# Kernel optimization log

Measured on AMD Instinct MI355X. Metric: run time of the kernel, lower is better.

The kernel has to match this reference:

```python
import jax, jax.numpy as jnp
import numpy as np

N = 50000  # nodes (spots)


def setup_inputs() -> dict:
    key = jax.random.key(0)
    ks = jax.random.split(key, 10)
    d_gene, d_img, H, Hh, O = 3000, 1024, 512, 256, 64

    def lin(k, i, o):
        return (jax.random.normal(k, (i, o), jnp.float32) / np.sqrt(i).astype(np.float32))

    return {
        "gene_data": jax.random.normal(ks[0], (N, d_gene), jnp.float32),
        "image_data": jax.random.normal(ks[1], (N, d_img), jnp.float32),
        "gene_edge_index": jax.random.randint(ks[2], (2, 800000), 0, N, dtype=jnp.int32).astype(jnp.int64),
        "spatial_edge_index": jax.random.randint(ks[3], (2, 300000), 0, N, dtype=jnp.int32).astype(jnp.int64),
        "W_fc1": lin(ks[4], d_gene, H), "b_fc1": jnp.zeros((H,), jnp.float32),
        "W_fc2": lin(ks[5], d_img, H), "b_fc2": jnp.zeros((H,), jnp.float32),
        "W_g11": lin(ks[6], H, Hh), "b_g11": jnp.zeros((Hh,), jnp.float32),
        "W_g12": lin(ks[7], H, Hh), "b_g12": jnp.zeros((Hh,), jnp.float32),
        "W_g21": lin(ks[8], Hh, O), "b_g21": jnp.zeros((O,), jnp.float32),
        "W_g22": lin(ks[9], Hh, O), "b_g22": jnp.zeros((O,), jnp.float32),
        "w1": jnp.float32(0.5), "w2": jnp.float32(0.5),
    }


def _gcn(x, edge_index, W, b, n):
    # PyG GCNConv: h = x @ W; add self-loops; symmetric norm D^-1/2 (A+I) D^-1/2; scatter-add; + bias
    h = x @ W  # [n, out]
    loop = jnp.arange(n, dtype=edge_index.dtype)
    src = jnp.concatenate([edge_index[0], loop])
    dst = jnp.concatenate([edge_index[1], loop])
    deg = jax.ops.segment_sum(jnp.ones_like(src, x.dtype), dst, num_segments=n)
    dinv = jax.lax.rsqrt(jnp.maximum(deg, jnp.asarray(1e-12, x.dtype)))
    norm = dinv[src] * dinv[dst]  # [E+n]
    out = jax.ops.segment_sum(h[src] * norm[:, None], dst, num_segments=n)
    return out + b


def reference(gene_data, image_data, gene_edge_index, spatial_edge_index,
              W_fc1, b_fc1, W_fc2, b_fc2,
              W_g11, b_g11, W_g12, b_g12,
              W_g21, b_g21, W_g22, b_g22,
              w1, w2):
    n = gene_data.shape[0]
    x1 = jax.nn.relu(gene_data @ W_fc1 + b_fc1)
    x2 = jax.nn.relu(image_data @ W_fc2 + b_fc2)
    # dropout: eval mode -> identity
    h1 = jax.nn.relu(_gcn(x1, spatial_edge_index, W_g11, b_g11, n))
    h2 = jax.nn.relu(_gcn(x2, gene_edge_index, W_g12, b_g12, n))
    x = w1 * h1 + (1.0 - w1) * h2
    o1 = _gcn(x, spatial_edge_index, W_g21, b_g21, n)
    o2 = _gcn(x, gene_edge_index, W_g22, b_g22, n)
    return w2 * o1 + (1.0 - w2) * o2
```

## Files before the change

### kernel.cpp

```cpp
#include <hip/hip_runtime.h>
#include <hip/hip_bf16.h>
#include <stdint.h>

typedef __attribute__((ext_vector_type(4))) float f32x4;
typedef __attribute__((ext_vector_type(8))) short short8;
typedef __attribute__((ext_vector_type(4))) short short4v;

#define CDIV(a, b) (((a) + (b) - 1) / (b))

__device__ __forceinline__ unsigned short f2bf(float x) {
  union { float f; unsigned int u; } c; c.f = x;
  unsigned int r = c.u + 0x7FFFu + ((c.u >> 16) & 1u);
  return (unsigned short)(r >> 16);
}
__device__ __forceinline__ unsigned short f2bf_hw(float x) {
  __hip_bfloat16 h = __float2bfloat16(x);
  unsigned short u; __builtin_memcpy(&u, &h, 2); return u;
}
__device__ __forceinline__ float bf2f(unsigned short b) {
  union { unsigned int u; float f; } c; c.u = (unsigned int)b << 16; return c.f;
}

__device__ __forceinline__ void gl2lds16(const void* g, void* lds) {
  __builtin_amdgcn_global_load_lds(
      reinterpret_cast<const __attribute__((address_space(1))) unsigned int*>(
          reinterpret_cast<uintptr_t>(g)),
      reinterpret_cast<__attribute__((address_space(3))) unsigned int*>(
          reinterpret_cast<uintptr_t>(lds)),
      16, 0, 0);
}

__global__ void transpose_w(const float* __restrict__ W, unsigned short* __restrict__ Wt,
                            int K, int N, int Kpad) {
  __shared__ float tile[32][33];
  int kb = blockIdx.x * 32, nb = blockIdx.y * 32;
  int tx = threadIdx.x & 31, ty = threadIdx.x >> 5;
  for (int r = ty; r < 32; r += 8) {
    int k = kb + r, n = nb + tx;
    tile[r][tx] = (k < K && n < N) ? W[(size_t)k * N + n] : 0.f;
  }
  __syncthreads();
  for (int r = ty; r < 32; r += 8) {
    int n = nb + r, k = kb + tx;
    if (n < N && k < Kpad) Wt[(size_t)n * Kpad + k] = f2bf(tile[tx][r]);
  }
}

__global__ void prep_init(int* __restrict__ dA, int* __restrict__ dB,
                          int* __restrict__ cA, int* __restrict__ cB, int n) {
  int i = blockIdx.x * blockDim.x + threadIdx.x;
  if (i < n) { dA[i] = 1; dB[i] = 1; cA[i] = 0; cB[i] = 0; }
}

__global__ void deg_hist_both(const int* __restrict__ eiA, int EA, int* __restrict__ degA,
                              const int* __restrict__ eiB, int EB, int* __restrict__ degB, int n) {
  int e = blockIdx.x * blockDim.x + threadIdx.x;
  if (e < EA) {
    unsigned int d = (unsigned int)eiA[(size_t)EA + e];
    if (d < (unsigned int)n) atomicAdd(&degA[d], 1);
  } else if (e < EA + EB) {
    int e2 = e - EA;
    unsigned int d = (unsigned int)eiB[(size_t)EB + e2];
    if (d < (unsigned int)n) atomicAdd(&degB[d], 1);
  }
}

__global__ void dinv_both(const int* __restrict__ dA, float* __restrict__ vA,
                          const int* __restrict__ dB, float* __restrict__ vB, int n) {
  int i = blockIdx.x * blockDim.x + threadIdx.x;
  if (i < n) { vA[i] = rsqrtf((float)dA[i]); vB[i] = rsqrtf((float)dB[i]); }
}

__global__ void scan_rowptr_dual(const int* __restrict__ degA, int* __restrict__ rpA,
                                 const int* __restrict__ degB, int* __restrict__ rpB, int n) {
  const int* deg = (blockIdx.x == 0) ? degA : degB;
  int* rp = (blockIdx.x == 0) ? rpA : rpB;
  __shared__ int wsum[16];
  __shared__ int carry_s;
  const int tid = threadIdx.x, lane = tid & 63, w = tid >> 6;
  if (tid == 0) carry_s = 0;
  __syncthreads();
  for (int base = 0; base < n; base += 1024) {
    int i = base + tid;
    int d = (i < n) ? (deg[i] - 1) : 0;
    int v = d;
    #pragma unroll
    for (int off = 1; off < 64; off <<= 1) {
      int t = __shfl_up(v, off, 64);
      if (lane >= off) v += t;
    }
    if (lane == 63) wsum[w] = v;
    __syncthreads();
    int carry = carry_s;
    if (w == 0) {
      int s = (lane < 16) ? wsum[lane] : 0;
      #pragma unroll
      for (int off = 1; off < 16; off <<= 1) {
        int t = __shfl_up(s, off, 64);
        if (lane >= off) s += t;
      }
      if (lane < 16) wsum[lane] = s;
    }
    __syncthreads();
    int woff = (w > 0) ? wsum[w - 1] : 0;
    if (i < n) rp[i] = carry + woff + v - d;
    if (tid == 0) carry_s = carry + wsum[15];
    __syncthreads();
  }
  if (threadIdx.x == 0) rp[n] = carry_s;
}

__global__ void csr_fill_both(const int* __restrict__ eiA, int EA, const int* __restrict__ rpA,
                              int* __restrict__ curA, const float* __restrict__ dvA,
                              int* __restrict__ csA, float* __restrict__ cnA,
                              const int* __restrict__ eiB, int EB, const int* __restrict__ rpB,
                              int* __restrict__ curB, const float* __restrict__ dvB,
                              int* __restrict__ csB, float* __restrict__ cnB, int n) {
  int e = blockIdx.x * blockDim.x + threadIdx.x;
  if (e < EA) {
    unsigned int s = (unsigned int)eiA[e];
    unsigned int d = (unsigned int)eiA[(size_t)EA + e];
    if (s < (unsigned int)n && d < (unsigned int)n) {
      int pos = rpA[d] + atomicAdd(&curA[d], 1);
      csA[pos] = (int)s;
      cnA[pos] = dvA[s] * dvA[d];
    }
  } else if (e < EA + EB) {
    int e2 = e - EA;
    unsigned int s = (unsigned int)eiB[e2];
    unsigned int d = (unsigned int)eiB[(size_t)EB + e2];
    if (s < (unsigned int)n && d < (unsigned int)n) {
      int pos = rpB[d] + atomicAdd(&curB[d], 1);
      csB[pos] = (int)s;
      cnB[pos] = dvB[s] * dvB[d];
    }
  }
}

template<int BM, int BN, int TH, int NT_N, int AMODE, bool ADD_BIAS, bool DO_RELU>
__global__ __launch_bounds__(TH, 2)
void gemm_pair(const void* __restrict__ A0, const unsigned short* __restrict__ Bt0,
               const float* __restrict__ b0, unsigned short* __restrict__ C0, int K0, int Kp0,
               const void* __restrict__ A1, const unsigned short* __restrict__ Bt1,
               const float* __restrict__ b1, unsigned short* __restrict__ C1, int K1, int Kp1,
               int split, int NT_M, int M, int N) {
  constexpr int BK = 64;
  constexpr int WN = TH / 64;
  constexpr int WCOLS = BN / WN;
  constexpr int FM = BM / 16, FN = WCOLS / 16;
  constexpr int BIT  = (BN * 8) / TH;
  constexpr int AIT1 = (BM * 8) / TH;
  constexpr int AIT3 = (BM * 16) / TH;
  constexpr int LOGN = (NT_N == 4) ? 2 : (NT_N == 2 ? 1 : 0);

  const int bid0 = blockIdx.x;
  const bool j1 = (bid0 >= split);
  const int bid = j1 ? (bid0 - split) : bid0;
  const void* Av = j1 ? A1 : A0;
  const unsigned short* Bt = j1 ? Bt1 : Bt0;
  const float* bias = j1 ? b1 : b0;
  unsigned short* C = j1 ? C1 : C0;
  const int K = j1 ? K1 : K0;
  const int Kpad = j1 ? Kp1 : Kp0;

  const int xcd = bid & 7, j = bid >> 3;
  const int per = (NT_M + 7) >> 3;
  const int mt = xcd * per + (j >> LOGN);
  const int nt = j & (NT_N - 1);
  if (mt >= NT_M) return;
  const int gm = mt * BM, gn = nt * BN;

  constexpr int ABYTES = (AMODE == 3) ? BM * BK * 4 : BM * BK * 2;
  __shared__ __align__(16) char AldsRaw[ABYTES];
  __shared__ __align__(16) unsigned short Blds[BN * BK];

  const int tid = threadIdx.x;
  const int wid = tid >> 6, lane = tid & 63;
  const int kg = lane >> 4, lr = lane & 15;
  const int sx = lr & 7;

  f32x4 acc[FM][FN] = {};

  const int nkt = Kpad / BK;
  for (int kt = 0; kt < nkt; ++kt) {
    const int k0 = kt * BK;
    if constexpr (AMODE == 1) {
      const unsigned short* A = (const unsigned short*)Av;
      unsigned short* Alds = (unsigned short*)AldsRaw;
      #pragma unroll
      for (int it = 0; it < AIT1; ++it) {
        int q = it * TH + tid;
        int r = q >> 3, s = q & 7;
        int grow = gm + r; if (grow > M - 1) grow = M - 1;
        gl2lds16(A + (size_t)grow * K + k0 + ((s ^ (r & 7)) << 3), &Alds[q * 8]);
      }
    } else {
      const float* A = (const float*)Av;
      float* Af = (float*)AldsRaw;
      if (k0 + BK <= K) {
        #pragma unroll
        for (int it = 0; it < AIT3; ++it) {
          int q = it * TH + tid;
          int r = q >> 4, s = q & 15;
          int grow = gm + r; if (grow > M - 1) grow = M - 1;
          gl2lds16(A + (size_t)grow * K + k0 + ((s ^ (r & 15)) << 2), &Af[q * 4]);
        }
      } else {
        #pragma unroll
        for (int it = 0; it < AIT3; ++it) {
          int q = it * TH + tid;
          int r = q >> 4, s = q & 15;
          int grow = gm + r; if (grow > M - 1) grow = M - 1;
          int kbase = k0 + ((s ^ (r & 15)) << 2);
          f32x4 v = {0.f, 0.f, 0.f, 0.f};
          if (kbase + 4 <= K) v = *(const f32x4*)(A + (size_t)grow * K + kbase);
          *(f32x4*)(&Af[q * 4]) = v;
        }
      }
    }
    #pragma unroll
    for (int it = 0; it < BIT; ++it) {
      int q = it * TH + tid;
      int r = q >> 3, s = q & 7;
      gl2lds16(Bt + (size_t)(gn + r) * Kpad + k0 + ((s ^ (r & 7)) << 3), &Blds[q * 8]);
    }
    __syncthreads();
    #pragma unroll
    for (int ks = 0; ks < 2; ++ks) {
      const int k8 = ks * 4 + kg;
      short8 af[FM];
      #pragma unroll
      for (int m = 0; m < FM; m++) {
        int r = m * 16 + lr;
        if constexpr (AMODE == 1) {
          const unsigned short* Alds = (const unsigned short*)AldsRaw;
          af[m] = *(const short8*)(&Alds[(r * 8 + (k8 ^ sx)) * 8]);
        } else {
          const float* Af = (const float*)AldsRaw;
          int s0 = (2 * k8) ^ lr, s1 = (2 * k8 + 1) ^ lr;
          f32x4 lo = *(const f32x4*)(Af + r * 64 + s0 * 4);
          f32x4 hi = *(const f32x4*)(Af + r * 64 + s1 * 4);
          #pragma unroll
          for (int i = 0; i < 4; i++) {
            af[m][i]     = (short)f2bf_hw(lo[i]);
            af[m][i + 4] = (short)f2bf_hw(hi[i]);
          }
        }
      }
      #pragma unroll
      for (int n2 = 0; n2 < FN; n2++) {
        int cc = wid * WCOLS + n2 * 16 + lr;
        short8 bq = *(const short8*)(&Blds[(cc * 8 + (k8 ^ sx)) * 8]);
        #pragma unroll
        for (int m = 0; m < FM; m++)
          acc[m][n2] = __builtin_amdgcn_mfma_f32_16x16x32_bf16(af[m], bq, acc[m][n2], 0, 0, 0);
      }
    }
    __syncthreads();
  }
  #pragma unroll
  for (int m = 0; m < FM; m++) {
    #pragma unroll
    for (int jj = 0; jj < 4; jj++) {
      int grow = gm + m * 16 + kg * 4 + jj;
      if (grow < M) {
        #pragma unroll
        for (int n2 = 0; n2 < FN; n2++) {
          int gcol = gn + wid * WCOLS + n2 * 16 + lr;
          float v = acc[m][n2][jj];
          if constexpr (ADD_BIAS) v += bias[gcol];
          if constexpr (DO_RELU) v = fmaxf(v, 0.f);
          C[(size_t)grow * N + gcol] = f2bf(v);
        }
      }
    }
  }
}

template<int BM, int BN, int TH, int NT_N, int AMODE, bool ADD_BIAS, bool DO_RELU>
__global__ __launch_bounds__(TH, 2)
void gemm7(const void* __restrict__ Av, const unsigned short* __restrict__ Bt,
           const float* __restrict__ bias, unsigned short* __restrict__ C,
           int NT_M, int M, int N, int K, int Kpad) {
  constexpr int BK = 64;
  constexpr int WN = TH / 64;
  constexpr int WCOLS = BN / WN;
  constexpr int FM = BM / 16, FN = WCOLS / 16;
  constexpr int BIT  = (BN * 8) / TH;
  constexpr int AIT1 = (BM * 8) / TH;
  constexpr int LOGN = (NT_N == 2) ? 1 : 0;

  const int bid = blockIdx.x;
  const int xcd = bid & 7, j = bid >> 3;
  const int per = (NT_M + 7) >> 3;
  const int mt = xcd * per + (j >> LOGN);
  const int nt = j & (NT_N - 1);
  if (mt >= NT_M) return;
  const int gm = mt * BM, gn = nt * BN;

  __shared__ __align__(16) unsigned short Alds[BM * BK];
  __shared__ __align__(16) unsigned short Blds[BN * BK];

  const int tid = threadIdx.x;
  const int wid = tid >> 6, lane = tid & 63;
  const int kg = lane >> 4, lr = lane & 15;
  const int sx = lr & 7;

  f32x4 acc[FM][FN] = {};

  const int nkt = Kpad / BK;
  for (int kt = 0; kt < nkt; ++kt) {
    const int k0 = kt * BK;
    const unsigned short* A = (const unsigned short*)Av;
    #pragma unroll
    for (int it = 0; it < AIT1; ++it) {
      int q = it * TH + tid;
      int r = q >> 3, s = q & 7;
      int grow = gm + r; if (grow > M - 1) grow = M - 1;
      gl2lds16(A + (size_t)grow * K + k0 + ((s ^ (r & 7)) << 3), &Alds[q * 8]);
    }
    #pragma unroll
    for (int it = 0; it < BIT; ++it) {
      int q = it * TH + tid;
      int r = q >> 3, s = q & 7;
      gl2lds16(Bt + (size_t)(gn + r) * Kpad + k0 + ((s ^ (r & 7)) << 3), &Blds[q * 8]);
    }
    __syncthreads();
    #pragma unroll
    for (int ks = 0; ks < 2; ++ks) {
      const int k8 = ks * 4 + kg;
      short8 af[FM];
      #pragma unroll
      for (int m = 0; m < FM; m++) {
        int r = m * 16 + lr;
        af[m] = *(const short8*)(&Alds[(r * 8 + (k8 ^ sx)) * 8]);
      }
      #pragma unroll
      for (int n2 = 0; n2 < FN; n2++) {
        int cc = wid * WCOLS + n2 * 16 + lr;
        short8 bq = *(const short8*)(&Blds[(cc * 8 + (k8 ^ sx)) * 8]);
        #pragma unroll
        for (int m = 0; m < FM; m++)
          acc[m][n2] = __builtin_amdgcn_mfma_f32_16x16x32_bf16(af[m], bq, acc[m][n2], 0, 0, 0);
      }
    }
    __syncthreads();
  }
  #pragma unroll
  for (int m = 0; m < FM; m++) {
    #pragma unroll
    for (int jj = 0; jj < 4; jj++) {
      int grow = gm + m * 16 + kg * 4 + jj;
      if (grow < M) {
        #pragma unroll
        for (int n2 = 0; n2 < FN; n2++) {
          int gcol = gn + wid * WCOLS + n2 * 16 + lr;
          float v = acc[m][n2][jj];
          if constexpr (ADD_BIAS) v += bias[gcol];
          if constexpr (DO_RELU) v = fmaxf(v, 0.f);
          C[(size_t)grow * N + gcol] = f2bf(v);
        }
      }
    }
  }
}

template<int LDH>
__device__ __forceinline__ f32x4 gcn_gather(const unsigned short* __restrict__ h,
                                            const int* __restrict__ rp,
                                            const int* __restrict__ cs,
                                            const float* __restrict__ cn,
                                            const float* __restrict__ dv,
                                            int node, int c4) {
  float d = dv[node];
  float sc = d * d;
  f32x4 a0, a1 = {0.f,0.f,0.f,0.f}, a2 = {0.f,0.f,0.f,0.f}, a3 = {0.f,0.f,0.f,0.f};
  {
    short4v v = *(const short4v*)(h + (size_t)node * LDH + c4);
    a0[0] = sc * bf2f((unsigned short)v[0]);
    a0[1] = sc * bf2f((unsigned short)v[1]);
    a0[2] = sc * bf2f((unsigned short)v[2]);
    a0[3] = sc * bf2f((unsigned short)v[3]);
  }
  int e = rp[node];
  const int e1 = rp[node + 1];
  for (; e + 4 <= e1; e += 4) {
    int s0 = cs[e], s1 = cs[e+1], s2 = cs[e+2], s3 = cs[e+3];
    float n0 = cn[e], n1 = cn[e+1], n2 = cn[e+2], n3 = cn[e+3];
    short4v v0 = *(const short4v*)(h + (size_t)s0 * LDH + c4);
    short4v v1 = *(const short4v*)(h + (size_t)s1 * LDH + c4);
    short4v v2 = *(const short4v*)(h + (size_t)s2 * LDH + c4);
    short4v v3 = *(const short4v*)(h + (size_t)s3 * LDH + c4);
    #pragma unroll
    for (int i = 0; i < 4; i++) {
      a0[i] += n0 * bf2f((unsigned short)v0[i]);
      a1[i] += n1 * bf2f((unsigned short)v1[i]);
      a2[i] += n2 * bf2f((unsigned short)v2[i]);
      a3[i] += n3 * bf2f((unsigned short)v3[i]);
    }
  }
  for (; e < e1; ++e) {
    int s0 = cs[e]; float n0 = cn[e];
    short4v v0 = *(const short4v*)(h + (size_t)s0 * LDH + c4);
    #pragma unroll
    for (int i = 0; i < 4; i++) a0[i] += n0 * bf2f((unsigned short)v0[i]);
  }
  #pragma unroll
  for (int i = 0; i < 4; i++) a0[i] += a1[i] + a2[i] + a3[i];
  return a0;
}

template<int F, int LDHA, int LDHB, bool DO_RELU, bool OUT_BF16>
__global__ __launch_bounds__(256)
void scatter_fused(const unsigned short* __restrict__ hA, const unsigned short* __restrict__ hB,
                   const int* __restrict__ rpA, const int* __restrict__ csA,
                   const float* __restrict__ cnA, const float* __restrict__ dvA,
                   const float* __restrict__ bA,
                   const int* __restrict__ rpB, const int* __restrict__ csB,
                   const float* __restrict__ cnB, const float* __restrict__ dvB,
                   const float* __restrict__ bB,
                   const float* __restrict__ wptr, void* __restrict__ outp, int n) {
  constexpr int TPN = F / 4;
  const int tid = threadIdx.x;
  const int node = blockIdx.x * (256 / TPN) + tid / TPN;
  const int c4 = (tid % TPN) * 4;
  if (node >= n) return;

  f32x4 accA = gcn_gather<LDHA>(hA, rpA, csA, cnA, dvA, node, c4);
  f32x4 accB = gcn_gather<LDHB>(hB, rpB, csB, cnB, dvB, node, c4);

  f32x4 bvA = *(const f32x4*)(bA + c4);
  f32x4 bvB = *(const f32x4*)(bB + c4);
  float w = *wptr;
  size_t idx = (size_t)node * F + c4;
  f32x4 r;
  #pragma unroll
  for (int i = 0; i < 4; i++) {
    float va = accA[i] + bvA[i];
    float vb = accB[i] + bvB[i];
    if constexpr (DO_RELU) { va = fmaxf(va, 0.f); vb = fmaxf(vb, 0.f); }
    r[i] = w * va + (1.f - w) * vb;
  }
  if constexpr (OUT_BF16) {
    short4v o;
    o[0] = (short)f2bf(r[0]); o[1] = (short)f2bf(r[1]);
    o[2] = (short)f2bf(r[2]); o[3] = (short)f2bf(r[3]);
    *(short4v*)((unsigned short*)outp + idx) = o;
  } else {
    *(f32x4*)((float*)outp + idx) = r;
  }
}

extern "C" void kernel_launch(void* const* d_in, const int* in_sizes, int n_in,
                              void* d_out, int out_size, void* d_ws, size_t ws_size,
                              hipStream_t stream) {
  const float* gene  = (const float*)d_in[0];
  const float* img   = (const float*)d_in[1];
  const int* ei_ge = (const int*)d_in[2];
  const int* ei_sp = (const int*)d_in[3];
  const float* W_fc1 = (const float*)d_in[4];  const float* b_fc1 = (const float*)d_in[5];
  const float* W_fc2 = (const float*)d_in[6];  const float* b_fc2 = (const float*)d_in[7];
  const float* W_g11 = (const float*)d_in[8];  const float* b_g11 = (const float*)d_in[9];
  const float* W_g12 = (const float*)d_in[10]; const float* b_g12 = (const float*)d_in[11];
  const float* W_g21 = (const float*)d_in[12]; const float* b_g21 = (const float*)d_in[13];
  const float* W_g22 = (const float*)d_in[14]; const float* b_g22 = (const float*)d_in[15];
  const float* w1p   = (const float*)d_in[16];
  const float* w2p   = (const float*)d_in[17];

  const int Nn = 50000;
  const int E_ge = in_sizes[2] / 2;
  const int E_sp = in_sizes[3] / 2;
  const int NT_M = CDIV(Nn, 64);
  const int PER  = CDIV(NT_M, 8);
  const int G1   = 8 * PER;
  const int G2   = 8 * PER * 2;

  char* ws = (char*)d_ws;
  size_t off = 0;
  auto alloc = [&](size_t bytes) -> void* {
    void* p = ws + off;
    off += (bytes + 255) & ~(size_t)255;
    return p;
  };

  unsigned short* Wt1  = (unsigned short*)alloc((size_t)512 * 3008 * 2);
  unsigned short* Wt2  = (unsigned short*)alloc((size_t)512 * 1024 * 2);
  unsigned short* Wt11 = (unsigned short*)alloc((size_t)256 * 512 * 2);
  unsigned short* Wt12 = (unsigned short*)alloc((size_t)256 * 512 * 2);
  unsigned short* WtC  = (unsigned short*)alloc((size_t)128 * 256 * 2);
  int*   deg_sp  = (int*)alloc((size_t)Nn * 4);
  int*   deg_ge  = (int*)alloc((size_t)Nn * 4);
  float* dinv_sp = (float*)alloc((size_t)Nn * 4);
  float* dinv_ge = (float*)alloc((size_t)Nn * 4);
  int*   rp_sp   = (int*)alloc((size_t)(Nn + 1) * 4);
  int*   rp_ge   = (int*)alloc((size_t)(Nn + 1) * 4);
  int*   cur_sp  = (int*)alloc((size_t)Nn * 4);
  int*   cur_ge  = (int*)alloc((size_t)Nn * 4);
  int*   csrc_sp = (int*)alloc((size_t)E_sp * 4);
  float* cnrm_sp = (float*)alloc((size_t)E_sp * 4);
  int*   csrc_ge = (int*)alloc((size_t)E_ge * 4);
  float* cnrm_ge = (float*)alloc((size_t)E_ge * 4);
  unsigned short* xbuf1 = (unsigned short*)alloc((size_t)Nn * 512 * 2);
  unsigned short* xbuf2 = (unsigned short*)alloc((size_t)Nn * 512 * 2);
  unsigned short* tmpA  = (unsigned short*)alloc((size_t)Nn * 256 * 2);
  unsigned short* tmpB  = (unsigned short*)alloc((size_t)Nn * 256 * 2);
  unsigned short* Xc    = xbuf1;
  unsigned short* tmp2  = tmpA;
  (void)ws_size; (void)n_in; (void)out_size;

  transpose_w<<<dim3(94, 16), 256, 0, stream>>>(W_fc1, Wt1, 3000, 512, 3008);
  transpose_w<<<dim3(32, 16), 256, 0, stream>>>(W_fc2, Wt2, 1024, 512, 1024);
  transpose_w<<<dim3(16, 8),  256, 0, stream>>>(W_g11, Wt11, 512, 256, 512);
  transpose_w<<<dim3(16, 8),  256, 0, stream>>>(W_g12, Wt12, 512, 256, 512);
  transpose_w<<<dim3(8, 2),   256, 0, stream>>>(W_g21, WtC, 256, 64, 256);
  transpose_w<<<dim3(8, 2),   256, 0, stream>>>(W_g22, WtC + (size_t)64 * 256, 256, 64, 256);

  prep_init<<<CDIV(Nn, 256), 256, 0, stream>>>(deg_sp, deg_ge, cur_sp, cur_ge, Nn);
  deg_hist_both<<<CDIV(E_sp + E_ge, 256), 256, 0, stream>>>(
      ei_sp, E_sp, deg_sp, ei_ge, E_ge, deg_ge, Nn);
  dinv_both<<<CDIV(Nn, 256), 256, 0, stream>>>(deg_sp, dinv_sp, deg_ge, dinv_ge, Nn);
  scan_rowptr_dual<<<2, 1024, 0, stream>>>(deg_sp, rp_sp, deg_ge, rp_ge, Nn);
  csr_fill_both<<<CDIV(E_sp + E_ge, 256), 256, 0, stream>>>(
      ei_sp, E_sp, rp_sp, cur_sp, dinv_sp, csrc_sp, cnrm_sp,
      ei_ge, E_ge, rp_ge, cur_ge, dinv_ge, csrc_ge, cnrm_ge, Nn);

  gemm_pair<64, 256, 256, 2, 3, true, true><<<2 * G2, 256, 0, stream>>>(
      gene, Wt1, b_fc1, xbuf1, 3000, 3008,
      img,  Wt2, b_fc2, xbuf2, 1024, 1024,
      G2, NT_M, Nn, 512);
  gemm_pair<64, 256, 256, 1, 1, false, false><<<2 * G1, 256, 0, stream>>>(
      xbuf1, Wt11, nullptr, tmpA, 512, 512,
      xbuf2, Wt12, nullptr, tmpB, 512, 512,
      G1, NT_M, Nn, 256);
  scatter_fused<256, 256, 256, true, true><<<Nn / 4, 256, 0, stream>>>(
      tmpA, tmpB, rp_sp, csrc_sp, cnrm_sp, dinv_sp, b_g11,
      rp_ge, csrc_ge, cnrm_ge, dinv_ge, b_g12, w1p, Xc, Nn);
  gemm7<64, 128, 256, 1, 1, false, false><<<G1, 256, 0, stream>>>(
      Xc, WtC, nullptr, tmp2, NT_M, Nn, 128, 256, 256);
  scatter_fused<64, 128, 128, false, false><<<Nn / 16, 256, 0, stream>>>(
      tmp2, tmp2 + 64, rp_sp, csrc_sp, cnrm_sp, dinv_sp, b_g21,
      rp_ge, csrc_ge, cnrm_ge, dinv_ge, b_g22, w2p, d_out, Nn);
}
```

Baseline: 736.7 us.

## Fold graph preprocessing into GEMM launches as tail blocks and merge transposes

The degree histogram now runs as extra tail blocks of the first GEMM launch, and the CSR fill runs as tail blocks of the second GEMM launch, so the atomic-heavy graph preprocessing overlaps with dense matrix work. The six weight transposes become a single launch that dispatches by block index. This removes several kernel launches and the serialization between them. The tail blocks share the GEMM's launch bounds and register allocation, and their scheduling relative to the GEMM tiles is not controlled.

```diff
diff --git a/kernel.cpp b/kernel.cpp
--- a/kernel.cpp
+++ b/kernel.cpp
@@ -30,10 +30,10 @@
       16, 0, 0);
 }
 
-__global__ void transpose_w(const float* __restrict__ W, unsigned short* __restrict__ Wt,
-                            int K, int N, int Kpad) {
+__device__ __forceinline__ void tr_tile(const float* __restrict__ W, unsigned short* __restrict__ Wt,
+                                        int K, int N, int Kpad, int bx, int by) {
   __shared__ float tile[32][33];
-  int kb = blockIdx.x * 32, nb = blockIdx.y * 32;
+  int kb = bx * 32, nb = by * 32;
   int tx = threadIdx.x & 31, ty = threadIdx.x >> 5;
   for (int r = ty; r < 32; r += 8) {
     int k = kb + r, n = nb + tx;
@@ -46,23 +46,26 @@
   }
 }
 
+__global__ __launch_bounds__(256)
+void transpose_all(const float* __restrict__ Wfc1, unsigned short* __restrict__ Wt1,
+                   const float* __restrict__ Wfc2, unsigned short* __restrict__ Wt2,
+                   const float* __restrict__ Wg11, unsigned short* __restrict__ Wt11,
+                   const float* __restrict__ Wg12, unsigned short* __restrict__ Wt12,
+                   const float* __restrict__ Wg21, const float* __restrict__ Wg22,
+                   unsigned short* __restrict__ WtC) {
+  int b = blockIdx.x;
+  if (b < 1504)      { tr_tile(Wfc1, Wt1, 3000, 512, 3008, b % 94, b / 94); }
+  else if (b < 2016) { int r = b - 1504; tr_tile(Wfc2, Wt2, 1024, 512, 1024, r % 32, r / 32); }
+  else if (b < 2144) { int r = b - 2016; tr_tile(Wg11, Wt11, 512, 256, 512, r % 16, r / 16); }
+  else if (b < 2272) { int r = b - 2144; tr_tile(Wg12, Wt12, 512, 256, 512, r % 16, r / 16); }
+  else if (b < 2288) { int r = b - 2272; tr_tile(Wg21, WtC, 256, 64, 256, r % 8, r / 8); }
+  else               { int r = b - 2288; tr_tile(Wg22, WtC + (size_t)64 * 256, 256, 64, 256, r % 8, r / 8); }
+}
+
 __global__ void prep_init(int* __restrict__ dA, int* __restrict__ dB,
                           int* __restrict__ cA, int* __restrict__ cB, int n) {
   int i = blockIdx.x * blockDim.x + threadIdx.x;
   if (i < n) { dA[i] = 1; dB[i] = 1; cA[i] = 0; cB[i] = 0; }
-}
-
-__global__ void deg_hist_both(const int* __restrict__ eiA, int EA, int* __restrict__ degA,
-                              const int* __restrict__ eiB, int EB, int* __restrict__ degB, int n) {
-  int e = blockIdx.x * blockDim.x + threadIdx.x;
-  if (e < EA) {
-    unsigned int d = (unsigned int)eiA[(size_t)EA + e];
-    if (d < (unsigned int)n) atomicAdd(&degA[d], 1);
-  } else if (e < EA + EB) {
-    int e2 = e - EA;
-    unsigned int d = (unsigned int)eiB[(size_t)EB + e2];
-    if (d < (unsigned int)n) atomicAdd(&degB[d], 1);
-  }
 }
 
 __global__ void dinv_both(const int* __restrict__ dA, float* __restrict__ vA,
@@ -110,40 +113,25 @@
   if (threadIdx.x == 0) rp[n] = carry_s;
 }
 
-__global__ void csr_fill_both(const int* __restrict__ eiA, int EA, const int* __restrict__ rpA,
-                              int* __restrict__ curA, const float* __restrict__ dvA,
-                              int* __restrict__ csA, float* __restrict__ cnA,
-                              const int* __restrict__ eiB, int EB, const int* __restrict__ rpB,
-                              int* __restrict__ curB, const float* __restrict__ dvB,
-                              int* __restrict__ csB, float* __restrict__ cnB, int n) {
-  int e = blockIdx.x * blockDim.x + threadIdx.x;
-  if (e < EA) {
-    unsigned int s = (unsigned int)eiA[e];
-    unsigned int d = (unsigned int)eiA[(size_t)EA + e];
-    if (s < (unsigned int)n && d < (unsigned int)n) {
-      int pos = rpA[d] + atomicAdd(&curA[d], 1);
-      csA[pos] = (int)s;
-      cnA[pos] = dvA[s] * dvA[d];
-    }
-  } else if (e < EA + EB) {
-    int e2 = e - EA;
-    unsigned int s = (unsigned int)eiB[e2];
-    unsigned int d = (unsigned int)eiB[(size_t)EB + e2];
-    if (s < (unsigned int)n && d < (unsigned int)n) {
-      int pos = rpB[d] + atomicAdd(&curB[d], 1);
-      csB[pos] = (int)s;
-      cnB[pos] = dvB[s] * dvB[d];
-    }
-  }
-}
-
-template<int BM, int BN, int TH, int NT_N, int AMODE, bool ADD_BIAS, bool DO_RELU>
+struct PrepArgs {
+  const int* eiA; int EA;
+  const int* eiB; int EB;
+  int n;
+  int* degA; int* degB;
+  const int* rpA; const int* rpB;
+  int* curA; int* curB;
+  const float* dvA; const float* dvB;
+  int* csA; float* cnA;
+  int* csB; float* cnB;
+};
+
+template<int BM, int BN, int TH, int NT_N, int AMODE, int TAIL, bool ADD_BIAS, bool DO_RELU>
 __global__ __launch_bounds__(TH, 2)
 void gemm_pair(const void* __restrict__ A0, const unsigned short* __restrict__ Bt0,
                const float* __restrict__ b0, unsigned short* __restrict__ C0, int K0, int Kp0,
                const void* __restrict__ A1, const unsigned short* __restrict__ Bt1,
                const float* __restrict__ b1, unsigned short* __restrict__ C1, int K1, int Kp1,
-               int split, int NT_M, int M, int N) {
+               int split, int NT_M, int M, int N, PrepArgs pa) {
   constexpr int BK = 64;
   constexpr int WN = TH / 64;
   constexpr int WCOLS = BN / WN;
@@ -154,6 +142,44 @@
   constexpr int LOGN = (NT_N == 4) ? 2 : (NT_N == 2 ? 1 : 0);
 
   const int bid0 = blockIdx.x;
+  const int tid = threadIdx.x;
+
+  if constexpr (TAIL != 0) {
+    if (bid0 >= 2 * split) {
+      int e = (bid0 - 2 * split) * TH + tid;
+      if constexpr (TAIL == 1) {
+        if (e < pa.EA) {
+          unsigned int d = (unsigned int)pa.eiA[(size_t)pa.EA + e];
+          if (d < (unsigned int)pa.n) atomicAdd(&pa.degA[d], 1);
+        } else if (e < pa.EA + pa.EB) {
+          int e2 = e - pa.EA;
+          unsigned int d = (unsigned int)pa.eiB[(size_t)pa.EB + e2];
+          if (d < (unsigned int)pa.n) atomicAdd(&pa.degB[d], 1);
+        }
+      } else {
+        if (e < pa.EA) {
+          unsigned int s = (unsigned int)pa.eiA[e];
+          unsigned int d = (unsigned int)pa.eiA[(size_t)pa.EA + e];
+          if (s < (unsigned int)pa.n && d < (unsigned int)pa.n) {
+            int pos = pa.rpA[d] + atomicAdd(&pa.curA[d], 1);
+            pa.csA[pos] = (int)s;
+            pa.cnA[pos] = pa.dvA[s] * pa.dvA[d];
+          }
+        } else if (e < pa.EA + pa.EB) {
+          int e2 = e - pa.EA;
+          unsigned int s = (unsigned int)pa.eiB[e2];
+          unsigned int d = (unsigned int)pa.eiB[(size_t)pa.EB + e2];
+          if (s < (unsigned int)pa.n && d < (unsigned int)pa.n) {
+            int pos = pa.rpB[d] + atomicAdd(&pa.curB[d], 1);
+            pa.csB[pos] = (int)s;
+            pa.cnB[pos] = pa.dvB[s] * pa.dvB[d];
+          }
+        }
+      }
+      return;
+    }
+  }
+
   const bool j1 = (bid0 >= split);
   const int bid = j1 ? (bid0 - split) : bid0;
   const void* Av = j1 ? A1 : A0;
@@ -174,7 +200,6 @@
   __shared__ __align__(16) char AldsRaw[ABYTES];
   __shared__ __align__(16) unsigned short Blds[BN * BK];
 
-  const int tid = threadIdx.x;
   const int wid = tid >> 6, lane = tid & 63;
   const int kg = lane >> 4, lr = lane & 15;
   const int sx = lr & 7;
@@ -474,6 +499,7 @@
   const int PER  = CDIV(NT_M, 8);
   const int G1   = 8 * PER;
   const int G2   = 8 * PER * 2;
+  const int TB   = CDIV(E_sp + E_ge, 256);
 
   char* ws = (char*)d_ws;
   size_t off = 0;
@@ -508,35 +534,43 @@
   unsigned short* tmp2  = tmpA;
   (void)ws_size; (void)n_in; (void)out_size;
 
-  transpose_w<<<dim3(94, 16), 256, 0, stream>>>(W_fc1, Wt1, 3000, 512, 3008);
-  transpose_w<<<dim3(32, 16), 256, 0, stream>>>(W_fc2, Wt2, 1024, 512, 1024);
-  transpose_w<<<dim3(16, 8),  256, 0, stream>>>(W_g11, Wt11, 512, 256, 512);
-  transpose_w<<<dim3(16, 8),  256, 0, stream>>>(W_g12, Wt12, 512, 256, 512);
-  transpose_w<<<dim3(8, 2),   256, 0, stream>>>(W_g21, WtC, 256, 64, 256);
-  transpose_w<<<dim3(8, 2),   256, 0, stream>>>(W_g22, WtC + (size_t)64 * 256, 256, 64, 256);
+  PrepArgs pa;
+  pa.eiA = ei_sp; pa.EA = E_sp;
+  pa.eiB = ei_ge; pa.EB = E_ge;
+  pa.n = Nn;
+  pa.degA = deg_sp; pa.degB = deg_ge;
+  pa.rpA = rp_sp; pa.rpB = rp_ge;
+  pa.curA = cur_sp; pa.curB = cur_ge;
+  pa.dvA = dinv_sp; pa.dvB = dinv_ge;
+  pa.csA = csrc_sp; pa.cnA = cnrm_sp;
+  pa.csB = csrc_ge; pa.cnB = cnrm_ge;
+
+  transpose_all<<<2304, 256, 0, stream>>>(W_fc1, Wt1, W_fc2, Wt2,
+                                          W_g11, Wt11, W_g12, Wt12,
+                                          W_g21, W_g22, WtC);
 
   prep_init<<<CDIV(Nn, 256), 256, 0, stream>>>(deg_sp, deg_ge, cur_sp, cur_ge, Nn);
-  deg_hist_both<<<CDIV(E_sp + E_ge, 256), 256, 0, stream>>>(
-      ei_sp, E_sp, deg_sp, ei_ge, E_ge, deg_ge, Nn);
+
+  gemm_pair<64, 256, 256, 2, 3, 1, true, true><<<2 * G2 + TB, 256, 0, stream>>>(
+      gene, Wt1, b_fc1, xbuf1, 3000, 3008,
+      img,  Wt2, b_fc2, xbuf2, 1024, 1024,
+      G2, NT_M, Nn, 512, pa);
+
   dinv_both<<<CDIV(Nn, 256), 256, 0, stream>>>(deg_sp, dinv_sp, deg_ge, dinv_ge, Nn);
   scan_rowptr_dual<<<2, 1024, 0, stream>>>(deg_sp, rp_sp, deg_ge, rp_ge, Nn);
-  csr_fill_both<<<CDIV(E_sp + E_ge, 256), 256, 0, stream>>>(
-      ei_sp, E_sp, rp_sp, cur_sp, dinv_sp, csrc_sp, cnrm_sp,
-      ei_ge, E_ge, rp_ge, cur_ge, dinv_ge, csrc_ge, cnrm_ge, Nn);
-
-  gemm_pair<64, 256, 256, 2, 3, true, true><<<2 * G2, 256, 0, stream>>>(
-      gene, Wt1, b_fc1, xbuf1, 3000, 3008,
-      img,  Wt2, b_fc2, xbuf2, 1024, 1024,
-      G2, NT_M, Nn, 512);
-  gemm_pair<64, 256, 256, 1, 1, false, false><<<2 * G1, 256, 0, stream>>>(
+
+  gemm_pair<64, 256, 256, 1, 1, 2, false, false><<<2 * G1 + TB, 256, 0, stream>>>(
       xbuf1, Wt11, nullptr, tmpA, 512, 512,
       xbuf2, Wt12, nullptr, tmpB, 512, 512,
-      G1, NT_M, Nn, 256);
+      G1, NT_M, Nn, 256, pa);
+
   scatter_fused<256, 256, 256, true, true><<<Nn / 4, 256, 0, stream>>>(
       tmpA, tmpB, rp_sp, csrc_sp, cnrm_sp, dinv_sp, b_g11,
       rp_ge, csrc_ge, cnrm_ge, dinv_ge, b_g12, w1p, Xc, Nn);
+
   gemm7<64, 128, 256, 1, 1, false, false><<<G1, 256, 0, stream>>>(
       Xc, WtC, nullptr, tmp2, NT_M, Nn, 128, 256, 256);
+
   scatter_fused<64, 128, 128, false, false><<<Nn / 16, 256, 0, stream>>>(
       tmp2, tmp2 + 64, rp_sp, csrc_sp, cnrm_sp, dinv_sp, b_g21,
       rp_ge, csrc_ge, cnrm_ge, dinv_ge, b_g22, w2p, d_out, Nn);
```

After: 674.6 us, median of 2. -8.4%, faster.
